# Performance work log

Measured on AMD Instinct MI355X. Metric: run time of the kernel, lower is better.

## Reference

```python
import jax, jax.numpy as jnp
import numpy as np

DIM = 1024
NUM_HEADS = 16
HEAD_DIM = DIM // NUM_HEADS
SCALE = HEAD_DIM ** -0.5


def setup_inputs() -> dict:
    key = jax.random.key(0)
    k_x, k_qkv, k_proj, k_pb = jax.random.split(key, 4)
    B, N = 4, 2048
    x = jax.random.normal(k_x, (B, N, DIM), dtype=jnp.float32)
    # qkv: Linear(dim, 3*dim), qkv_bias=False -> no bias
    W_qkv = jax.random.normal(k_qkv, (DIM, 3 * DIM), dtype=jnp.float32) * (DIM ** -0.5)
    # proj: Linear(dim, dim) with bias (nn.Linear default)
    W_proj = jax.random.normal(k_proj, (DIM, DIM), dtype=jnp.float32) * (DIM ** -0.5)
    b_proj = jax.random.normal(k_pb, (DIM,), dtype=jnp.float32) * 0.01
    return {"x": x, "W_qkv": W_qkv, "W_proj": W_proj, "b_proj": b_proj}


def reference(x, W_qkv, W_proj, b_proj):
    B, N, C = x.shape
    H, D = NUM_HEADS, HEAD_DIM
    # qkv projection -> [B, N, 3, H, D] -> q,k,v each [B, H, N, D]
    qkv = (x @ W_qkv).reshape(B, N, 3, H, D)
    q, k, v = (jnp.moveaxis(qkv, 2, 0).transpose(0, 1, 3, 2, 4))  # [3,B,H,N,D]
    # attention scores [B, H, N, N], scaled QK^T (full matrix, as in source)
    attn = jnp.einsum('bhqd,bhkd->bhqk', q, k) * SCALE
    attn = jax.nn.softmax(attn, axis=-1)
    # attn @ V -> [B, H, N, D] -> [B, N, C]
    out = jnp.einsum('bhqk,bhkd->bhqd', attn, v)
    out = out.transpose(0, 2, 1, 3).reshape(B, N, C)
    # output projection
    return out @ W_proj + b_proj
```

## Files before the change

### kernel.cpp

```cpp
#include <hip/hip_runtime.h>
#include <hip/hip_bf16.h>

typedef __attribute__((ext_vector_type(8))) short short8;
typedef __attribute__((ext_vector_type(4))) short short4_t;
typedef __attribute__((ext_vector_type(4))) float floatx4;
typedef unsigned short u16;
typedef unsigned int u32;

#define SEQ 2048
#define NH 16
#define HD 64
#define CDIM 1024
#define MTOT 8192

__device__ __forceinline__ u16 f2bf(float f) {
  u32 u = __builtin_bit_cast(u32, f);
  u32 r = u + 0x7FFFu + ((u >> 16) & 1u);
  return (u16)(r >> 16);
}

__device__ __forceinline__ void gload16(const void* g, void* l) {
  __builtin_amdgcn_global_load_lds(
      (const __attribute__((address_space(1))) u32*)g,
      (__attribute__((address_space(3))) u32*)l, 16, 0, 0);
}

__global__ void cvt_x_kernel(const float* __restrict__ x, u16* __restrict__ xb) {
  size_t i = (size_t)blockIdx.x * 256 + threadIdx.x;
  const float4* xv = (const float4*)x;
  float4 a = xv[2 * i], c = xv[2 * i + 1];
  union { u16 h[8]; short8 v; } u;
  u.h[0] = f2bf(a.x); u.h[1] = f2bf(a.y); u.h[2] = f2bf(a.z); u.h[3] = f2bf(a.w);
  u.h[4] = f2bf(c.x); u.h[5] = f2bf(c.y); u.h[6] = f2bf(c.z); u.h[7] = f2bf(c.w);
  *(short8*)(xb + 8 * i) = u.v;
}

__global__ void transpose_w(const float* __restrict__ w, u16* __restrict__ wt,
                            int K, int N) {
  __shared__ float t[32][33];
  int n0 = blockIdx.x * 32, k0 = blockIdx.y * 32;
  int tr = threadIdx.x >> 5, tc = threadIdx.x & 31;
#pragma unroll
  for (int i = 0; i < 4; i++) {
    int r = tr + i * 8;
    t[r][tc] = w[(size_t)(k0 + r) * N + n0 + tc];
  }
  __syncthreads();
#pragma unroll
  for (int i = 0; i < 4; i++) {
    int r = tr + i * 8;
    wt[(size_t)(n0 + r) * K + k0 + tc] = f2bf(t[tc][r]);
  }
}

__global__ __launch_bounds__(256, 2) void gemm_qkv(
    const u16* __restrict__ A, const u16* __restrict__ BT,
    u16* __restrict__ qb, u16* __restrict__ kb, u16* __restrict__ vtb) {
  __shared__ u16 Ab[128 * 32];
  __shared__ u16 Bb[128 * 32];
  const int tid = threadIdx.x;
  const int w = tid >> 6, l = tid & 63;
  const int quad = l >> 4, l15 = l & 15;
  const int m0 = blockIdx.x * 128, n0 = blockIdx.y * 128;
  const int wr = w >> 1, wc = w & 1;

  floatx4 acc[4][4] = {};

  for (int k0 = 0; k0 < 1024; k0 += 32) {
    __syncthreads();
#pragma unroll
    for (int rnd = 0; rnd < 2; rnd++) {
      int ci = rnd * 256 + tid;
      int r = ci >> 2, pos = ci & 3;
      int c = pos ^ ((r >> 1) & 3);
      gload16(A + (size_t)(m0 + r) * 1024 + k0 + c * 8, (char*)Ab + ci * 16);
      gload16(BT + (size_t)(n0 + r) * 1024 + k0 + c * 8, (char*)Bb + ci * 16);
    }
    __syncthreads();
    short8 af[4], bf[4];
#pragma unroll
    for (int t = 0; t < 4; t++) {
      int ra = wr * 64 + t * 16 + l15;
      af[t] = *(short8*)((char*)Ab + ra * 64 + (quad ^ ((ra >> 1) & 3)) * 16);
      int rb = wc * 64 + t * 16 + l15;
      bf[t] = *(short8*)((char*)Bb + rb * 64 + (quad ^ ((rb >> 1) & 3)) * 16);
    }
#pragma unroll
    for (int i = 0; i < 4; i++)
#pragma unroll
      for (int j = 0; j < 4; j++)
        acc[i][j] = __builtin_amdgcn_mfma_f32_16x16x32_bf16(af[i], bf[j], acc[i][j], 0, 0, 0);
  }

#pragma unroll
  for (int i = 0; i < 4; i++)
#pragma unroll
    for (int j = 0; j < 4; j++)
#pragma unroll
      for (int r = 0; r < 4; r++) {
        int m = m0 + wr * 64 + i * 16 + quad * 4 + r;
        int c = n0 + wc * 64 + j * 16 + l15;
        int b = m >> 11, n = m & 2047;
        int t = c >> 10, rem = c & 1023;
        int h = rem >> 6, d = rem & 63;
        int bh = b * NH + h;
        if (t == 0)      qb[((size_t)bh * SEQ + n) * HD + d] = f2bf(acc[i][j][r] * 0.18033688011112042f);
        else if (t == 1) kb[((size_t)bh * SEQ + n) * HD + d] = f2bf(acc[i][j][r]);
        else             vtb[((size_t)bh * HD + d) * SEQ + n] = f2bf(acc[i][j][r]);
      }
}

__global__ __launch_bounds__(256, 2) void gemm_proj(
    const u16* __restrict__ A, const u16* __restrict__ BT,
    const float* __restrict__ bias, float* __restrict__ out) {
  __shared__ u16 Ab[128 * 32];
  __shared__ u16 Bb[128 * 32];
  const int tid = threadIdx.x;
  const int w = tid >> 6, l = tid & 63;
  const int quad = l >> 4, l15 = l & 15;
  const int m0 = blockIdx.x * 128, n0 = blockIdx.y * 128;
  const int wr = w >> 1, wc = w & 1;

  floatx4 acc[4][4] = {};

  for (int k0 = 0; k0 < 1024; k0 += 32) {
    __syncthreads();
#pragma unroll
    for (int rnd = 0; rnd < 2; rnd++) {
      int ci = rnd * 256 + tid;
      int r = ci >> 2, pos = ci & 3;
      int c = pos ^ ((r >> 1) & 3);
      gload16(A + (size_t)(m0 + r) * 1024 + k0 + c * 8, (char*)Ab + ci * 16);
      gload16(BT + (size_t)(n0 + r) * 1024 + k0 + c * 8, (char*)Bb + ci * 16);
    }
    __syncthreads();
    short8 af[4], bf[4];
#pragma unroll
    for (int t = 0; t < 4; t++) {
      int ra = wr * 64 + t * 16 + l15;
      af[t] = *(short8*)((char*)Ab + ra * 64 + (quad ^ ((ra >> 1) & 3)) * 16);
      int rb = wc * 64 + t * 16 + l15;
      bf[t] = *(short8*)((char*)Bb + rb * 64 + (quad ^ ((rb >> 1) & 3)) * 16);
    }
#pragma unroll
    for (int i = 0; i < 4; i++)
#pragma unroll
      for (int j = 0; j < 4; j++)
        acc[i][j] = __builtin_amdgcn_mfma_f32_16x16x32_bf16(af[i], bf[j], acc[i][j], 0, 0, 0);
  }

#pragma unroll
  for (int i = 0; i < 4; i++)
#pragma unroll
    for (int j = 0; j < 4; j++)
#pragma unroll
      for (int r = 0; r < 4; r++) {
        int m = m0 + wr * 64 + i * 16 + quad * 4 + r;
        int c = n0 + wc * 64 + j * 16 + l15;
        out[(size_t)m * CDIM + c] = acc[i][j][r] + bias[c];
      }
}

__global__ __launch_bounds__(256, 2) void attn_kernel(
    const u16* __restrict__ Qb, const u16* __restrict__ Kb,
    const u16* __restrict__ Vtb, u16* __restrict__ attnb) {
  __shared__ char smem[65536];
  const int tid = threadIdx.x;
  const int w = tid >> 6, l = tid & 63;
  const int quad = l >> 4, l15 = l & 15;

  const int lb = blockIdx.x + (blockIdx.y << 3);
  const int bh = ((lb & 7) << 3) + ((lb >> 3) & 7);
  const int qt0 = (lb >> 6) * 256;

  const u16* Kbase = Kb + (size_t)bh * SEQ * HD;
  const u16* Vbase = Vtb + (size_t)bh * HD * SEQ;

  short8 qf[4][2];
#pragma unroll
  for (int rt = 0; rt < 4; rt++) {
    int qrow = qt0 + w * 64 + rt * 16 + l15;
#pragma unroll
    for (int ks = 0; ks < 2; ks++)
      qf[rt][ks] = *(const short8*)(Qb + ((size_t)bh * SEQ + qrow) * HD + ks * 32 + quad * 8);
  }

  floatx4 O[4][4] = {};
  floatx4 sumacc[4] = {};

  union { u16 h[8]; short8 v; } onesu;
#pragma unroll
  for (int z = 0; z < 8; z++) onesu.h[z] = 0x3F80;
  const short8 ones = onesu.v;

  auto stage = [&](int n0, char* base) {
#pragma unroll
    for (int rnd = 0; rnd < 4; rnd++) {
      int ci = rnd * 256 + tid;
      int r = ci >> 3, pos = ci & 7;
      int c = pos ^ ((r & 7) ^ ((r >> 1) & 4));
      gload16(Kbase + (size_t)(n0 + r) * HD + c * 8, base + ci * 16);
    }
#pragma unroll
    for (int rnd = 0; rnd < 4; rnd++) {
      int ci = rnd * 256 + tid;
      int r = ci >> 4, pos = ci & 15;
      int c = pos ^ (r & 15);
      gload16(Vbase + (size_t)r * SEQ + n0 + c * 8, base + 16384 + ci * 16);
    }
  };

  stage(0, smem);
  __syncthreads();

  for (int kt = 0; kt < 16; kt++) {
    char* cur = smem + (kt & 1) * 32768;
    if (kt < 15) stage((kt + 1) * 128, smem + ((kt + 1) & 1) * 32768);

    char* KtC = cur;
    char* VtsC = cur + 16384;
#pragma unroll
    for (int p = 0; p < 4; p++) {
      floatx4 s[2][4];
#pragma unroll
      for (int t = 0; t < 2; t++) {
        int rho = p * 32 + (l15 >> 2) * 8 + t * 4 + (l15 & 3);
        int g = (rho & 7) ^ ((rho >> 1) & 4);
        short8 kf0 = *(short8*)(KtC + rho * 128 + ((0 + quad) ^ g) * 16);
        short8 kf1 = *(short8*)(KtC + rho * 128 + ((4 + quad) ^ g) * 16);
#pragma unroll
        for (int rt = 0; rt < 4; rt++) {
          floatx4 z = {};
          z = __builtin_amdgcn_mfma_f32_16x16x32_bf16(kf0, qf[rt][0], z, 0, 0, 0);
          z = __builtin_amdgcn_mfma_f32_16x16x32_bf16(kf1, qf[rt][1], z, 0, 0, 0);
          s[t][rt] = z;
        }
      }
      short8 pf[4];
#pragma unroll
      for (int rt = 0; rt < 4; rt++) {
        union { u32 d[4]; short8 v; } pu;
#pragma unroll
        for (int t = 0; t < 2; t++) {
          float e0 = __builtin_amdgcn_exp2f(s[t][rt][0]);
          float e1 = __builtin_amdgcn_exp2f(s[t][rt][1]);
          float e2 = __builtin_amdgcn_exp2f(s[t][rt][2]);
          float e3 = __builtin_amdgcn_exp2f(s[t][rt][3]);
          pu.d[t * 2 + 0] = __builtin_amdgcn_perm(
              __builtin_bit_cast(u32, e1), __builtin_bit_cast(u32, e0), 0x07060302u);
          pu.d[t * 2 + 1] = __builtin_amdgcn_perm(
              __builtin_bit_cast(u32, e3), __builtin_bit_cast(u32, e2), 0x07060302u);
        }
        pf[rt] = pu.v;
        sumacc[rt] = __builtin_amdgcn_mfma_f32_16x16x32_bf16(ones, pf[rt], sumacc[rt], 0, 0, 0);
      }
#pragma unroll
      for (int dt = 0; dt < 4; dt++) {
        int rv = dt * 16 + l15;
        short8 vf = *(short8*)(VtsC + rv * 256 + ((p * 4 + quad) ^ (rv & 15)) * 16);
#pragma unroll
        for (int rt = 0; rt < 4; rt++)
          O[rt][dt] = __builtin_amdgcn_mfma_f32_16x16x32_bf16(vf, pf[rt], O[rt][dt], 0, 0, 0);
      }
    }
    __syncthreads();
  }

  float inv[4];
#pragma unroll
  for (int rt = 0; rt < 4; rt++) inv[rt] = 1.f / sumacc[rt][0];

#pragma unroll
  for (int rt = 0; rt < 4; rt++)
#pragma unroll
    for (int dt = 0; dt < 4; dt++) {
      union { u16 h[4]; short4_t v; } pk;
#pragma unroll
      for (int r = 0; r < 4; r++) pk.h[r] = f2bf(O[rt][dt][r] * inv[rt]);
      *(short4_t*)(smem + (w * 64 + rt * 16 + l15) * 144 + (dt * 16 + quad * 4) * 2) = pk.v;
    }
  __syncthreads();
  {
    const int b = bh >> 4, h = bh & 15;
#pragma unroll
    for (int it = 0; it < 2; it++) {
      int row = it * 128 + (tid >> 1);
      int half = tid & 1;
      u16* gp = attnb + ((size_t)(b * SEQ + qt0 + row)) * CDIM + h * 64 + half * 32;
      char* lp = smem + row * 144 + half * 64;
#pragma unroll
      for (int c = 0; c < 4; c++)
        *(short8*)(gp + c * 8) = *(short8*)(lp + c * 16);
    }
  }
}

extern "C" void kernel_launch(void* const* d_in, const int* in_sizes, int n_in,
                              void* d_out, int out_size, void* d_ws, size_t ws_size,
                              hipStream_t stream) {
  const float* x = (const float*)d_in[0];
  const float* Wqkv = (const float*)d_in[1];
  const float* Wproj = (const float*)d_in[2];
  const float* bproj = (const float*)d_in[3];
  float* out = (float*)d_out;

  u16* xb = (u16*)d_ws;
  u16* wqkvT = xb + (size_t)8388608;
  u16* wprojT = wqkvT + (size_t)3145728;
  u16* qb = wprojT + (size_t)1048576;
  u16* kb = qb + (size_t)8388608;
  u16* vtb = kb + (size_t)8388608;
  u16* attnb = xb;

  cvt_x_kernel<<<4096, 256, 0, stream>>>(x, xb);
  transpose_w<<<dim3(96, 32), 256, 0, stream>>>(Wqkv, wqkvT, 1024, 3072);
  transpose_w<<<dim3(32, 32), 256, 0, stream>>>(Wproj, wprojT, 1024, 1024);
  gemm_qkv<<<dim3(64, 24), 256, 0, stream>>>(xb, wqkvT, qb, kb, vtb);
  attn_kernel<<<dim3(8, 64), 256, 0, stream>>>(qb, kb, vtb, attnb);
  gemm_proj<<<dim3(64, 8), 256, 0, stream>>>(attnb, wprojT, bproj, out);
}
```

Baseline: 263.3 us.

## Double GEMM K-tile to 64 and compute softmax row sums with VALU adds

Both projection GEMMs now stage a 64-wide K slice per iteration, using an 8-way XOR swizzle, which halves the number of barrier pairs and loop iterations. Each wave issues twice as many MFMAs per sync, at the cost of more LDS per block. In the attention kernel, the row-sum MFMA against a ones vector is replaced by per-lane fp32 accumulation of the exponentials, reduced across quads with two shuffles at the end. This frees MFMA issue slots and sums the unrounded fp32 values instead of the bf16-rounded ones.

```diff
diff --git a/kernel.cpp b/kernel.cpp
--- a/kernel.cpp
+++ b/kernel.cpp
@@ -56,8 +56,8 @@
 __global__ __launch_bounds__(256, 2) void gemm_qkv(
     const u16* __restrict__ A, const u16* __restrict__ BT,
     u16* __restrict__ qb, u16* __restrict__ kb, u16* __restrict__ vtb) {
-  __shared__ u16 Ab[128 * 32];
-  __shared__ u16 Bb[128 * 32];
+  __shared__ u16 Ab[128 * 64];
+  __shared__ u16 Bb[128 * 64];
   const int tid = threadIdx.x;
   const int w = tid >> 6, l = tid & 63;
   const int quad = l >> 4, l15 = l & 15;
@@ -66,30 +66,38 @@
 
   floatx4 acc[4][4] = {};
 
-  for (int k0 = 0; k0 < 1024; k0 += 32) {
-    __syncthreads();
-#pragma unroll
-    for (int rnd = 0; rnd < 2; rnd++) {
+  for (int k0 = 0; k0 < 1024; k0 += 64) {
+    __syncthreads();
+#pragma unroll
+    for (int rnd = 0; rnd < 4; rnd++) {
       int ci = rnd * 256 + tid;
-      int r = ci >> 2, pos = ci & 3;
-      int c = pos ^ ((r >> 1) & 3);
+      int r = ci >> 3, pos = ci & 7;
+      int c = pos ^ (r & 7);
       gload16(A + (size_t)(m0 + r) * 1024 + k0 + c * 8, (char*)Ab + ci * 16);
       gload16(BT + (size_t)(n0 + r) * 1024 + k0 + c * 8, (char*)Bb + ci * 16);
     }
     __syncthreads();
-    short8 af[4], bf[4];
+    short8 af[4][2], bf[4][2];
 #pragma unroll
     for (int t = 0; t < 4; t++) {
       int ra = wr * 64 + t * 16 + l15;
-      af[t] = *(short8*)((char*)Ab + ra * 64 + (quad ^ ((ra >> 1) & 3)) * 16);
+      int ga = ra & 7;
+#pragma unroll
+      for (int ks = 0; ks < 2; ks++)
+        af[t][ks] = *(short8*)((char*)Ab + ra * 128 + ((ks * 4 + quad) ^ ga) * 16);
       int rb = wc * 64 + t * 16 + l15;
-      bf[t] = *(short8*)((char*)Bb + rb * 64 + (quad ^ ((rb >> 1) & 3)) * 16);
-    }
-#pragma unroll
-    for (int i = 0; i < 4; i++)
-#pragma unroll
-      for (int j = 0; j < 4; j++)
-        acc[i][j] = __builtin_amdgcn_mfma_f32_16x16x32_bf16(af[i], bf[j], acc[i][j], 0, 0, 0);
+      int gb = rb & 7;
+#pragma unroll
+      for (int ks = 0; ks < 2; ks++)
+        bf[t][ks] = *(short8*)((char*)Bb + rb * 128 + ((ks * 4 + quad) ^ gb) * 16);
+    }
+#pragma unroll
+    for (int ks = 0; ks < 2; ks++)
+#pragma unroll
+      for (int i = 0; i < 4; i++)
+#pragma unroll
+        for (int j = 0; j < 4; j++)
+          acc[i][j] = __builtin_amdgcn_mfma_f32_16x16x32_bf16(af[i][ks], bf[j][ks], acc[i][j], 0, 0, 0);
   }
 
 #pragma unroll
@@ -113,8 +121,8 @@
 __global__ __launch_bounds__(256, 2) void gemm_proj(
     const u16* __restrict__ A, const u16* __restrict__ BT,
     const float* __restrict__ bias, float* __restrict__ out) {
-  __shared__ u16 Ab[128 * 32];
-  __shared__ u16 Bb[128 * 32];
+  __shared__ u16 Ab[128 * 64];
+  __shared__ u16 Bb[128 * 64];
   const int tid = threadIdx.x;
   const int w = tid >> 6, l = tid & 63;
   const int quad = l >> 4, l15 = l & 15;
@@ -123,30 +131,38 @@
 
   floatx4 acc[4][4] = {};
 
-  for (int k0 = 0; k0 < 1024; k0 += 32) {
-    __syncthreads();
-#pragma unroll
-    for (int rnd = 0; rnd < 2; rnd++) {
+  for (int k0 = 0; k0 < 1024; k0 += 64) {
+    __syncthreads();
+#pragma unroll
+    for (int rnd = 0; rnd < 4; rnd++) {
       int ci = rnd * 256 + tid;
-      int r = ci >> 2, pos = ci & 3;
-      int c = pos ^ ((r >> 1) & 3);
+      int r = ci >> 3, pos = ci & 7;
+      int c = pos ^ (r & 7);
       gload16(A + (size_t)(m0 + r) * 1024 + k0 + c * 8, (char*)Ab + ci * 16);
       gload16(BT + (size_t)(n0 + r) * 1024 + k0 + c * 8, (char*)Bb + ci * 16);
     }
     __syncthreads();
-    short8 af[4], bf[4];
+    short8 af[4][2], bf[4][2];
 #pragma unroll
     for (int t = 0; t < 4; t++) {
       int ra = wr * 64 + t * 16 + l15;
-      af[t] = *(short8*)((char*)Ab + ra * 64 + (quad ^ ((ra >> 1) & 3)) * 16);
+      int ga = ra & 7;
+#pragma unroll
+      for (int ks = 0; ks < 2; ks++)
+        af[t][ks] = *(short8*)((char*)Ab + ra * 128 + ((ks * 4 + quad) ^ ga) * 16);
       int rb = wc * 64 + t * 16 + l15;
-      bf[t] = *(short8*)((char*)Bb + rb * 64 + (quad ^ ((rb >> 1) & 3)) * 16);
-    }
-#pragma unroll
-    for (int i = 0; i < 4; i++)
-#pragma unroll
-      for (int j = 0; j < 4; j++)
-        acc[i][j] = __builtin_amdgcn_mfma_f32_16x16x32_bf16(af[i], bf[j], acc[i][j], 0, 0, 0);
+      int gb = rb & 7;
+#pragma unroll
+      for (int ks = 0; ks < 2; ks++)
+        bf[t][ks] = *(short8*)((char*)Bb + rb * 128 + ((ks * 4 + quad) ^ gb) * 16);
+    }
+#pragma unroll
+    for (int ks = 0; ks < 2; ks++)
+#pragma unroll
+      for (int i = 0; i < 4; i++)
+#pragma unroll
+        for (int j = 0; j < 4; j++)
+          acc[i][j] = __builtin_amdgcn_mfma_f32_16x16x32_bf16(af[i][ks], bf[j][ks], acc[i][j], 0, 0, 0);
   }
 
 #pragma unroll
@@ -186,12 +202,7 @@
   }
 
   floatx4 O[4][4] = {};
-  floatx4 sumacc[4] = {};
-
-  union { u16 h[8]; short8 v; } onesu;
-#pragma unroll
-  for (int z = 0; z < 8; z++) onesu.h[z] = 0x3F80;
-  const short8 ones = onesu.v;
+  float lsum[4] = {0.f, 0.f, 0.f, 0.f};
 
   auto stage = [&](int n0, char* base) {
 #pragma unroll
@@ -240,19 +251,21 @@
 #pragma unroll
       for (int rt = 0; rt < 4; rt++) {
         union { u32 d[4]; short8 v; } pu;
+        float ls = lsum[rt];
 #pragma unroll
         for (int t = 0; t < 2; t++) {
           float e0 = __builtin_amdgcn_exp2f(s[t][rt][0]);
           float e1 = __builtin_amdgcn_exp2f(s[t][rt][1]);
           float e2 = __builtin_amdgcn_exp2f(s[t][rt][2]);
           float e3 = __builtin_amdgcn_exp2f(s[t][rt][3]);
+          ls += (e0 + e1) + (e2 + e3);
           pu.d[t * 2 + 0] = __builtin_amdgcn_perm(
               __builtin_bit_cast(u32, e1), __builtin_bit_cast(u32, e0), 0x07060302u);
           pu.d[t * 2 + 1] = __builtin_amdgcn_perm(
               __builtin_bit_cast(u32, e3), __builtin_bit_cast(u32, e2), 0x07060302u);
         }
+        lsum[rt] = ls;
         pf[rt] = pu.v;
-        sumacc[rt] = __builtin_amdgcn_mfma_f32_16x16x32_bf16(ones, pf[rt], sumacc[rt], 0, 0, 0);
       }
 #pragma unroll
       for (int dt = 0; dt < 4; dt++) {
@@ -268,7 +281,11 @@
 
   float inv[4];
 #pragma unroll
-  for (int rt = 0; rt < 4; rt++) inv[rt] = 1.f / sumacc[rt][0];
+  for (int rt = 0; rt < 4; rt++) {
+    lsum[rt] += __shfl_xor(lsum[rt], 16, 64);
+    lsum[rt] += __shfl_xor(lsum[rt], 32, 64);
+    inv[rt] = 1.f / lsum[rt];
+  }
 
 #pragma unroll
   for (int rt = 0; rt < 4; rt++)
```

Measured after the change: 389.9 us. 48.1% more time.
